# Kernel tuning notes

Measured on AMD Instinct MI355X. Metric: run time of the kernel, lower is better.

The kernel has to match this reference:

```python
import jax, jax.numpy as jnp
import numpy as np

INDIM = 128
OUTDIM = 256
GRID = 16


def setup_inputs() -> dict:
    key = jax.random.key(0)
    kx, kc = jax.random.split(key)
    x = jax.random.normal(kx, (32768, INDIM), dtype=jnp.float32)
    # fouriercoeffs: (2, outdim, indim, gridsize), init randn / (sqrt(indim)*sqrt(gridsize))
    fouriercoeffs = jax.random.normal(kc, (2, OUTDIM, INDIM, GRID), dtype=jnp.float32) / (
        np.sqrt(INDIM) * np.sqrt(GRID)
    )
    bias = jnp.zeros((1, OUTDIM), dtype=jnp.float32)
    return {"x": x, "fouriercoeffs": fouriercoeffs, "bias": bias}


def reference(x, fouriercoeffs, bias):
    orig_shape = x.shape
    x2 = x.reshape(-1, INDIM)  # (N, indim)
    k = jnp.arange(1, GRID + 1, dtype=x2.dtype)  # (gridsize,)
    x_scaled = x2[:, :, None] * k  # (N, indim, gridsize)
    y = (
        jnp.einsum("nig,oig->no", jnp.cos(x_scaled), fouriercoeffs[0])
        + jnp.einsum("nig,oig->no", jnp.sin(x_scaled), fouriercoeffs[1])
        + bias
    )
    return y.reshape(*orig_shape[:-1], OUTDIM)
```

## Files before the change

kernel.cpp:

```cpp
#include <hip/hip_runtime.h>
#include <cstdint>

#define IN_DIM   128
#define OUT_DIM  256
#define NROWS    32768
#define BM       64
#define NSTEPS   32
#define STR      65

typedef unsigned short u16;
typedef __attribute__((ext_vector_type(8)))  __bf16 bf16x8;
typedef __attribute__((ext_vector_type(16))) float  f32x16;

#define BARRIER_LGKM()                                         \
    do {                                                       \
        asm volatile("s_waitcnt lgkmcnt(0)" ::: "memory");     \
        __builtin_amdgcn_s_barrier();                          \
    } while (0)

__global__ __launch_bounds__(256) void kan_prep(const float* __restrict__ C,
                                                u16* __restrict__ Bpack) {
    const int o = threadIdx.x;
    const int i = blockIdx.x;
    const int t = blockIdx.y;
    const float* src = C + (((size_t)(t * OUT_DIM + o) * IN_DIM + i) * 16);
    bf16x8 lo = {}, hi = {};
#pragma unroll
    for (int g = 0; g < 8; ++g) {
        lo[g] = (__bf16)src[g];
        hi[g] = (__bf16)src[8 + g];
    }
    const int ko = i * 4 + t * 2;
    bf16x8* dst = (bf16x8*)Bpack;
    dst[(size_t)ko * OUT_DIM + o]       = lo;
    dst[(size_t)(ko + 1) * OUT_DIM + o] = hi;
}

__global__ __launch_bounds__(256, 2) void kan_gemm(const float* __restrict__ x,
                                                   const u16* __restrict__ Bpack,
                                                   const float* __restrict__ bias,
                                                   float* __restrict__ out) {
    __shared__ __align__(16) u16 Asm[2][16 * STR * 8];

    const int tid  = threadIdx.x;
    const int lane = tid & 63;
    const int wn   = tid >> 6;
    const int la31 = lane & 31;
    const int gh   = lane >> 5;
    const int m0   = blockIdx.x * BM;

    const int tr  = tid >> 2;
    const int til = tid & 3;

    f32x16 vz;
#pragma unroll
    for (int r = 0; r < 16; ++r) vz[r] = 0.f;
    f32x16 acc[2][2] = {{vz, vz}, {vz, vz}};

    const bf16x8* Bv = (const bf16x8*)Bpack;
    bf16x8* Av0 = (bf16x8*)Asm[0];
    bf16x8* Av1 = (bf16x8*)Asm[1];

    const float* xrow = x + (size_t)(m0 + tr) * IN_DIM + til;
    const int bcol = wn * 64 + la31;

    auto gen = [&](bf16x8* Av, float xv) {
        float s1, c1;
        __sincosf(xv, &s1, &c1);
        const float t2 = 2.f * c1;
        bf16x8 qc0 = {}, qc1 = {}, qs0 = {}, qs1 = {};
        float cp = c1, sp = s1;
        float cc = t2 * c1 - 1.f, sc = t2 * s1;
        qc0[0] = (__bf16)cp;  qs0[0] = (__bf16)sp;
        qc0[1] = (__bf16)cc;  qs0[1] = (__bf16)sc;
#pragma unroll
        for (int g = 3; g <= 16; ++g) {
            const float cn = t2 * cc - cp;
            const float sn = t2 * sc - sp;
            cp = cc; sp = sc; cc = cn; sc = sn;
            const int idx = g - 1;
            if (idx < 8) { qc0[idx] = (__bf16)cc;      qs0[idx] = (__bf16)sc; }
            else         { qc1[idx - 8] = (__bf16)cc;  qs1[idx - 8] = (__bf16)sc; }
        }
        const int kob = til * 4;
        Av[(kob + 0) * STR + tr] = qc0;
        Av[(kob + 1) * STR + tr] = qc1;
        Av[(kob + 2) * STR + tr] = qs0;
        Av[(kob + 3) * STR + tr] = qs1;
    };

    bf16x8 bA[8], bB[8];

#pragma unroll
    for (int j = 0; j < 4; ++j)
#pragma unroll
        for (int fn = 0; fn < 2; ++fn)
            bA[j * 2 + fn] = Bv[(size_t)((j >> 1) * 4 + (j & 1) * 2 + gh) * OUT_DIM
                                + bcol + fn * 32];
    float xn = xrow[4];
    gen(Av0, xrow[0]);
    BARRIER_LGKM();

    for (int kt = 0; kt < NSTEPS; ++kt) {
        bf16x8* Avc = (kt & 1) ? Av1 : Av0;
        bf16x8* Avn = (kt & 1) ? Av0 : Av1;

#pragma unroll
        for (int j = 0; j < 4; ++j)
#pragma unroll
            for (int fn = 0; fn < 2; ++fn)
                bB[j * 2 + fn] = Bv[(size_t)(kt * 16 + 8 + (j >> 1) * 4 + (j & 1) * 2 + gh)
                                    * OUT_DIM + bcol + fn * 32];

        if (kt + 1 < NSTEPS) {
            gen(Avn, xn);
            xn = xrow[((kt + 2) & (NSTEPS - 1)) * 4];
        }

#pragma unroll
        for (int j = 0; j < 4; ++j) {
            const int koL = (j >> 1) * 4 + (j & 1) * 2 + gh;
            const bf16x8 af0 = Avc[koL * STR + la31];
            const bf16x8 af1 = Avc[koL * STR + 32 + la31];
            acc[0][0] = __builtin_amdgcn_mfma_f32_32x32x16_bf16(af0, bA[j*2+0], acc[0][0], 0, 0, 0);
            acc[0][1] = __builtin_amdgcn_mfma_f32_32x32x16_bf16(af0, bA[j*2+1], acc[0][1], 0, 0, 0);
            acc[1][0] = __builtin_amdgcn_mfma_f32_32x32x16_bf16(af1, bA[j*2+0], acc[1][0], 0, 0, 0);
            acc[1][1] = __builtin_amdgcn_mfma_f32_32x32x16_bf16(af1, bA[j*2+1], acc[1][1], 0, 0, 0);
        }

        {
            const int ktn = (kt + 1) & (NSTEPS - 1);
#pragma unroll
            for (int j = 0; j < 4; ++j)
#pragma unroll
                for (int fn = 0; fn < 2; ++fn)
                    bA[j * 2 + fn] = Bv[(size_t)(ktn * 16 + (j >> 1) * 4 + (j & 1) * 2 + gh)
                                        * OUT_DIM + bcol + fn * 32];
        }

#pragma unroll
        for (int j = 0; j < 4; ++j) {
            const int koL = 8 + (j >> 1) * 4 + (j & 1) * 2 + gh;
            const bf16x8 af0 = Avc[koL * STR + la31];
            const bf16x8 af1 = Avc[koL * STR + 32 + la31];
            acc[0][0] = __builtin_amdgcn_mfma_f32_32x32x16_bf16(af0, bB[j*2+0], acc[0][0], 0, 0, 0);
            acc[0][1] = __builtin_amdgcn_mfma_f32_32x32x16_bf16(af0, bB[j*2+1], acc[0][1], 0, 0, 0);
            acc[1][0] = __builtin_amdgcn_mfma_f32_32x32x16_bf16(af1, bB[j*2+0], acc[1][0], 0, 0, 0);
            acc[1][1] = __builtin_amdgcn_mfma_f32_32x32x16_bf16(af1, bB[j*2+1], acc[1][1], 0, 0, 0);
        }
        BARRIER_LGKM();
    }

#pragma unroll
    for (int fn = 0; fn < 2; ++fn) {
        const int col = bcol + fn * 32;
        const float bv = bias[col];
#pragma unroll
        for (int fm = 0; fm < 2; ++fm) {
            const int rbase = m0 + fm * 32 + 4 * gh;
#pragma unroll
            for (int r = 0; r < 16; ++r) {
                const int row = rbase + (r & 3) + 8 * (r >> 2);
                out[(size_t)row * OUT_DIM + col] = acc[fm][fn][r] + bv;
            }
        }
    }
}

extern "C" void kernel_launch(void* const* d_in, const int* in_sizes, int n_in,
                              void* d_out, int out_size, void* d_ws, size_t ws_size,
                              hipStream_t stream) {
    const float* x    = (const float*)d_in[0];
    const float* fc   = (const float*)d_in[1];
    const float* bias = (const float*)d_in[2];
    float* out        = (float*)d_out;
    u16* Bpack        = (u16*)d_ws;

    kan_prep<<<dim3(IN_DIM, 2), OUT_DIM, 0, stream>>>(fc, Bpack);
    kan_gemm<<<dim3(NROWS / BM), 256, 0, stream>>>(x, Bpack, bias, out);
}
```

Measured before the change: 81.29 us.

## Split gemm block into producer waves for sincos generation and MFMA consumer waves

The block grows from 4 to 6 waves. Two extra producer waves compute the Chebyshev sin/cos features for all 64 rows, each thread handling two rows, and write them to LDS. The four consumer waves now only load B and issue MFMAs, so feature generation and matrix math can run on separate waves. In exchange the block uses more threads and registers, which may lower occupancy, and the consumers still wait on the producers at every k-step barrier.

```diff
diff --git a/kernel.cpp b/kernel.cpp
--- a/kernel.cpp
+++ b/kernel.cpp
@@ -36,7 +36,7 @@
     dst[(size_t)(ko + 1) * OUT_DIM + o] = hi;
 }
 
-__global__ __launch_bounds__(256, 2) void kan_gemm(const float* __restrict__ x,
+__global__ __launch_bounds__(384, 2) void kan_gemm(const float* __restrict__ x,
                                                    const u16* __restrict__ Bpack,
                                                    const float* __restrict__ bias,
                                                    float* __restrict__ out) {
@@ -44,13 +44,16 @@
 
     const int tid  = threadIdx.x;
     const int lane = tid & 63;
-    const int wn   = tid >> 6;
+    const int wid  = tid >> 6;
+    const bool isProd = (wid >= 4);
+    const int wn   = wid & 3;
     const int la31 = lane & 31;
     const int gh   = lane >> 5;
     const int m0   = blockIdx.x * BM;
 
-    const int tr  = tid >> 2;
-    const int til = tid & 3;
+    const int pid = tid - 256;
+    const int tr  = (pid >> 2) & 31;
+    const int til = pid & 3;
 
     f32x16 vz;
 #pragma unroll
@@ -61,10 +64,9 @@
     bf16x8* Av0 = (bf16x8*)Asm[0];
     bf16x8* Av1 = (bf16x8*)Asm[1];
 
-    const float* xrow = x + (size_t)(m0 + tr) * IN_DIM + til;
     const int bcol = wn * 64 + la31;
 
-    auto gen = [&](bf16x8* Av, float xv) {
+    auto gen = [&](bf16x8* Av, float xv, int trL) {
         float s1, c1;
         __sincosf(xv, &s1, &c1);
         const float t2 = 2.f * c1;
@@ -83,73 +85,89 @@
             else         { qc1[idx - 8] = (__bf16)cc;  qs1[idx - 8] = (__bf16)sc; }
         }
         const int kob = til * 4;
-        Av[(kob + 0) * STR + tr] = qc0;
-        Av[(kob + 1) * STR + tr] = qc1;
-        Av[(kob + 2) * STR + tr] = qs0;
-        Av[(kob + 3) * STR + tr] = qs1;
+        Av[(kob + 0) * STR + trL] = qc0;
+        Av[(kob + 1) * STR + trL] = qc1;
+        Av[(kob + 2) * STR + trL] = qs0;
+        Av[(kob + 3) * STR + trL] = qs1;
     };
+
+    const float* xP0 = x + (size_t)(m0 + tr) * IN_DIM + til;
+    const float* xP1 = xP0 + 32 * IN_DIM;
 
     bf16x8 bA[8], bB[8];
 
+    float xa = 0.f, xb = 0.f;
+    if (isProd) {
+        gen(Av0, xP0[0], tr);
+        gen(Av0, xP1[0], tr + 32);
+        xa = xP0[4];
+        xb = xP1[4];
+    } else {
 #pragma unroll
-    for (int j = 0; j < 4; ++j)
+        for (int j = 0; j < 4; ++j)
 #pragma unroll
-        for (int fn = 0; fn < 2; ++fn)
-            bA[j * 2 + fn] = Bv[(size_t)((j >> 1) * 4 + (j & 1) * 2 + gh) * OUT_DIM
-                                + bcol + fn * 32];
-    float xn = xrow[4];
-    gen(Av0, xrow[0]);
+            for (int fn = 0; fn < 2; ++fn)
+                bA[j * 2 + fn] = Bv[(size_t)((j >> 1) * 4 + (j & 1) * 2 + gh) * OUT_DIM
+                                    + bcol + fn * 32];
+    }
     BARRIER_LGKM();
 
     for (int kt = 0; kt < NSTEPS; ++kt) {
         bf16x8* Avc = (kt & 1) ? Av1 : Av0;
         bf16x8* Avn = (kt & 1) ? Av0 : Av1;
 
-#pragma unroll
-        for (int j = 0; j < 4; ++j)
-#pragma unroll
-            for (int fn = 0; fn < 2; ++fn)
-                bB[j * 2 + fn] = Bv[(size_t)(kt * 16 + 8 + (j >> 1) * 4 + (j & 1) * 2 + gh)
-                                    * OUT_DIM + bcol + fn * 32];
-
-        if (kt + 1 < NSTEPS) {
-            gen(Avn, xn);
-            xn = xrow[((kt + 2) & (NSTEPS - 1)) * 4];
-        }
-
-#pragma unroll
-        for (int j = 0; j < 4; ++j) {
-            const int koL = (j >> 1) * 4 + (j & 1) * 2 + gh;
-            const bf16x8 af0 = Avc[koL * STR + la31];
-            const bf16x8 af1 = Avc[koL * STR + 32 + la31];
-            acc[0][0] = __builtin_amdgcn_mfma_f32_32x32x16_bf16(af0, bA[j*2+0], acc[0][0], 0, 0, 0);
-            acc[0][1] = __builtin_amdgcn_mfma_f32_32x32x16_bf16(af0, bA[j*2+1], acc[0][1], 0, 0, 0);
-            acc[1][0] = __builtin_amdgcn_mfma_f32_32x32x16_bf16(af1, bA[j*2+0], acc[1][0], 0, 0, 0);
-            acc[1][1] = __builtin_amdgcn_mfma_f32_32x32x16_bf16(af1, bA[j*2+1], acc[1][1], 0, 0, 0);
-        }
-
-        {
-            const int ktn = (kt + 1) & (NSTEPS - 1);
+        if (isProd) {
+            if (kt + 1 < NSTEPS) {
+                gen(Avn, xa, tr);
+                gen(Avn, xb, tr + 32);
+                const int k2 = ((kt + 2) & (NSTEPS - 1)) * 4;
+                xa = xP0[k2];
+                xb = xP1[k2];
+            }
+        } else {
 #pragma unroll
             for (int j = 0; j < 4; ++j)
 #pragma unroll
                 for (int fn = 0; fn < 2; ++fn)
-                    bA[j * 2 + fn] = Bv[(size_t)(ktn * 16 + (j >> 1) * 4 + (j & 1) * 2 + gh)
+                    bB[j * 2 + fn] = Bv[(size_t)(kt * 16 + 8 + (j >> 1) * 4 + (j & 1) * 2 + gh)
                                         * OUT_DIM + bcol + fn * 32];
-        }
 
 #pragma unroll
-        for (int j = 0; j < 4; ++j) {
-            const int koL = 8 + (j >> 1) * 4 + (j & 1) * 2 + gh;
-            const bf16x8 af0 = Avc[koL * STR + la31];
-            const bf16x8 af1 = Avc[koL * STR + 32 + la31];
-            acc[0][0] = __builtin_amdgcn_mfma_f32_32x32x16_bf16(af0, bB[j*2+0], acc[0][0], 0, 0, 0);
-            acc[0][1] = __builtin_amdgcn_mfma_f32_32x32x16_bf16(af0, bB[j*2+1], acc[0][1], 0, 0, 0);
-            acc[1][0] = __builtin_amdgcn_mfma_f32_32x32x16_bf16(af1, bB[j*2+0], acc[1][0], 0, 0, 0);
-            acc[1][1] = __builtin_amdgcn_mfma_f32_32x32x16_bf16(af1, bB[j*2+1], acc[1][1], 0, 0, 0);
+            for (int j = 0; j < 4; ++j) {
+                const int koL = (j >> 1) * 4 + (j & 1) * 2 + gh;
+                const bf16x8 af0 = Avc[koL * STR + la31];
+                const bf16x8 af1 = Avc[koL * STR + 32 + la31];
+                acc[0][0] = __builtin_amdgcn_mfma_f32_32x32x16_bf16(af0, bA[j*2+0], acc[0][0], 0, 0, 0);
+                acc[0][1] = __builtin_amdgcn_mfma_f32_32x32x16_bf16(af0, bA[j*2+1], acc[0][1], 0, 0, 0);
+                acc[1][0] = __builtin_amdgcn_mfma_f32_32x32x16_bf16(af1, bA[j*2+0], acc[1][0], 0, 0, 0);
+                acc[1][1] = __builtin_amdgcn_mfma_f32_32x32x16_bf16(af1, bA[j*2+1], acc[1][1], 0, 0, 0);
+            }
+
+            {
+                const int ktn = (kt + 1) & (NSTEPS - 1);
+#pragma unroll
+                for (int j = 0; j < 4; ++j)
+#pragma unroll
+                    for (int fn = 0; fn < 2; ++fn)
+                        bA[j * 2 + fn] = Bv[(size_t)(ktn * 16 + (j >> 1) * 4 + (j & 1) * 2 + gh)
+                                            * OUT_DIM + bcol + fn * 32];
+            }
+
+#pragma unroll
+            for (int j = 0; j < 4; ++j) {
+                const int koL = 8 + (j >> 1) * 4 + (j & 1) * 2 + gh;
+                const bf16x8 af0 = Avc[koL * STR + la31];
+                const bf16x8 af1 = Avc[koL * STR + 32 + la31];
+                acc[0][0] = __builtin_amdgcn_mfma_f32_32x32x16_bf16(af0, bB[j*2+0], acc[0][0], 0, 0, 0);
+                acc[0][1] = __builtin_amdgcn_mfma_f32_32x32x16_bf16(af0, bB[j*2+1], acc[0][1], 0, 0, 0);
+                acc[1][0] = __builtin_amdgcn_mfma_f32_32x32x16_bf16(af1, bB[j*2+0], acc[1][0], 0, 0, 0);
+                acc[1][1] = __builtin_amdgcn_mfma_f32_32x32x16_bf16(af1, bB[j*2+1], acc[1][1], 0, 0, 0);
+            }
         }
         BARRIER_LGKM();
     }
+
+    if (isProd) return;
 
 #pragma unroll
     for (int fn = 0; fn < 2; ++fn) {
@@ -177,5 +195,5 @@
     u16* Bpack        = (u16*)d_ws;
 
     kan_prep<<<dim3(IN_DIM, 2), OUT_DIM, 0, stream>>>(fc, Bpack);
-    kan_gemm<<<dim3(NROWS / BM), 256, 0, stream>>>(x, Bpack, bias, out);
+    kan_gemm<<<dim3(NROWS / BM), 384, 0, stream>>>(x, Bpack, bias, out);
 }
```

Result: slower. 119.6 us (+47.1%).

## Split output columns across two 128-thread blocks per row tile

Applied to the files above, without the earlier changes.

Each block now covers half of the output columns (128) with two waves instead of all 256 columns with four waves, so twice as many blocks are launched. Each thread generates the sin/cos features for two rows, which means the feature generation for a 64-row tile is duplicated across the two blocks sharing it. The aim is smaller blocks for more scheduling flexibility and occupancy, at the cost of redundant trig work and a second read of x.

```diff
diff --git a/kernel.cpp b/kernel.cpp
--- a/kernel.cpp
+++ b/kernel.cpp
@@ -4,7 +4,6 @@
 #define IN_DIM   128
 #define OUT_DIM  256
 #define NROWS    32768
-#define BM       64
 #define NSTEPS   32
 #define STR      65
 
@@ -36,7 +35,7 @@
     dst[(size_t)(ko + 1) * OUT_DIM + o] = hi;
 }
 
-__global__ __launch_bounds__(256, 2) void kan_gemm(const float* __restrict__ x,
+__global__ __launch_bounds__(128, 2) void kan_gemm(const float* __restrict__ x,
                                                    const u16* __restrict__ Bpack,
                                                    const float* __restrict__ bias,
                                                    float* __restrict__ out) {
@@ -44,12 +43,14 @@
 
     const int tid  = threadIdx.x;
     const int lane = tid & 63;
-    const int wn   = tid >> 6;
+    const int wid  = tid >> 6;
     const int la31 = lane & 31;
     const int gh   = lane >> 5;
-    const int m0   = blockIdx.x * BM;
+    const int bid  = blockIdx.x;
+    const int wnb  = bid & 1;
+    const int m0   = (bid >> 1) * 64;
 
-    const int tr  = tid >> 2;
+    const int tr  = (tid >> 2) & 31;
     const int til = tid & 3;
 
     f32x16 vz;
@@ -61,10 +62,9 @@
     bf16x8* Av0 = (bf16x8*)Asm[0];
     bf16x8* Av1 = (bf16x8*)Asm[1];
 
-    const float* xrow = x + (size_t)(m0 + tr) * IN_DIM + til;
-    const int bcol = wn * 64 + la31;
+    const int bcol = wnb * 128 + wid * 64 + la31;
 
-    auto gen = [&](bf16x8* Av, float xv) {
+    auto gen = [&](bf16x8* Av, float xv, int trL) {
         float s1, c1;
         __sincosf(xv, &s1, &c1);
         const float t2 = 2.f * c1;
@@ -83,11 +83,14 @@
             else         { qc1[idx - 8] = (__bf16)cc;  qs1[idx - 8] = (__bf16)sc; }
         }
         const int kob = til * 4;
-        Av[(kob + 0) * STR + tr] = qc0;
-        Av[(kob + 1) * STR + tr] = qc1;
-        Av[(kob + 2) * STR + tr] = qs0;
-        Av[(kob + 3) * STR + tr] = qs1;
+        Av[(kob + 0) * STR + trL] = qc0;
+        Av[(kob + 1) * STR + trL] = qc1;
+        Av[(kob + 2) * STR + trL] = qs0;
+        Av[(kob + 3) * STR + trL] = qs1;
     };
+
+    const float* xr0 = x + (size_t)(m0 + tr) * IN_DIM + til;
+    const float* xr1 = xr0 + (size_t)32 * IN_DIM;
 
     bf16x8 bA[8], bB[8];
 
@@ -97,8 +100,10 @@
         for (int fn = 0; fn < 2; ++fn)
             bA[j * 2 + fn] = Bv[(size_t)((j >> 1) * 4 + (j & 1) * 2 + gh) * OUT_DIM
                                 + bcol + fn * 32];
-    float xn = xrow[4];
-    gen(Av0, xrow[0]);
+    float xa = xr0[0], xb = xr1[0];
+    float xan = xr0[4], xbn = xr1[4];
+    gen(Av0, xa, tr);
+    gen(Av0, xb, tr + 32);
     BARRIER_LGKM();
 
     for (int kt = 0; kt < NSTEPS; ++kt) {
@@ -113,8 +118,11 @@
                                     * OUT_DIM + bcol + fn * 32];
 
         if (kt + 1 < NSTEPS) {
-            gen(Avn, xn);
-            xn = xrow[((kt + 2) & (NSTEPS - 1)) * 4];
+            gen(Avn, xan, tr);
+            gen(Avn, xbn, tr + 32);
+            const int k2 = ((kt + 2) & (NSTEPS - 1)) * 4;
+            xan = xr0[k2];
+            xbn = xr1[k2];
         }
 
 #pragma unroll
@@ -177,5 +185,5 @@
     u16* Bpack        = (u16*)d_ws;
 
     kan_prep<<<dim3(IN_DIM, 2), OUT_DIM, 0, stream>>>(fc, Bpack);
-    kan_gemm<<<dim3(NROWS / BM), 256, 0, stream>>>(x, Bpack, bias, out);
+    kan_gemm<<<dim3(NROWS / 64 * 2), 128, 0, stream>>>(x, Bpack, bias, out);
 }
```

New measurement: 86.29 us. +6.1%, slower.
